# Kernel tuning notes

Hardware: AMD Instinct MI355X
Metric: run time of the kernel (lower is better)

Reference implementation:

```python
import jax, jax.numpy as jnp
import numpy as np
from jax import lax

WINDOW = 9
LOSS_WEIGHT = 1.0
EPS = 1e-05
BALANCE = 0.2

_DN = ('NCHW', 'OIHW', 'NCHW')

def _local_sum(x, k=WINDOW):
    # Separable box-filter sum == conv2d with ones((1,1,k,k)), padding=k//2.
    pad = k // 2
    kh = jnp.ones((1, 1, k, 1), x.dtype)
    kw = jnp.ones((1, 1, 1, k), x.dtype)
    y = lax.conv_general_dilated(x, kh, (1, 1), [(pad, pad), (0, 0)], dimension_numbers=_DN)
    return lax.conv_general_dilated(y, kw, (1, 1), [(0, 0), (pad, pad)], dimension_numbers=_DN)

def _lncc_loss(pred, target, k=WINDOW, eps=EPS):
    n = k * k
    pred_mean = _local_sum(pred, k) / n
    target_mean = _local_sum(target, k) / n
    # NOTE: faithful to source: variance uses raw local sum of squares minus mean^2
    pred_var = jnp.clip(_local_sum(pred * pred, k) - pred_mean * pred_mean, 0.0, None)
    target_var = jnp.clip(_local_sum(target * target, k) - target_mean * target_mean, 0.0, None)
    cov = _local_sum(pred * target, k) - pred_mean * target_mean
    lncc = cov / (jnp.sqrt(pred_var + eps) * jnp.sqrt(target_var + eps))
    return 1.0 - jnp.mean(lncc)

def setup_inputs() -> dict:
    key = jax.random.key(0)
    k1, k2, k3 = jax.random.split(key, 3)
    B, H, W = 16, 512, 512
    pred = jax.random.normal(k1, (B, 1, H, W), dtype=jnp.float32)
    target = jax.random.normal(k2, (B, 1, H, W), dtype=jnp.float32)
    mask = jax.random.normal(k3, (B, 2, H, W), dtype=jnp.float32)
    return {"pred": pred, "target": target, "mask": mask}

def reference(pred, target, mask):
    m = jnp.argmax(mask, axis=1)[:, None].astype(pred.dtype)  # [B,1,H,W]
    p_pred1 = (1.0 - m) * pred
    p_pred2 = (1.0 - m) * target
    n_pred1 = m * pred
    n_pred2 = m * target
    return LOSS_WEIGHT * (BALANCE * _lncc_loss(p_pred1, p_pred2)
                          - (1.0 - BALANCE) * _lncc_loss(n_pred1, n_pred2))
```

## Files before the change

### kernel.cpp

```cpp
#include <hip/hip_runtime.h>

#define NB   16
#define NH   512
#define NW   512
#define RAD  4
#define BH   4
#define NBANDS (NH / BH)
#define NBLOCKS (NB * NBANDS)
#define EPSF 1e-5f
#define SBYTES_PER_IMG (NH * NW / 8)
#define SBYTES_TOTAL   (NB * SBYTES_PER_IMG)

__device__ __forceinline__ float lncc_val(float Sa, float Sb, float Saa, float Sbb, float Sab) {
    const float inv_n = 1.0f / 81.0f;
    float ma  = Sa * inv_n;
    float mb  = Sb * inv_n;
    float va  = fmaxf(Saa - ma * ma, 0.0f);
    float vb  = fmaxf(Sbb - mb * mb, 0.0f);
    float cov = Sab - ma * mb;
    return cov * rsqrtf((va + EPSF) * (vb + EPSF));
}

__global__ __launch_bounds__(256)
void mask_pre(const float* __restrict__ mask, unsigned* __restrict__ sbits) {
    int tid = blockIdx.x * blockDim.x + threadIdx.x;
    const size_t hw = (size_t)NH * NW;
    size_t g0 = (size_t)tid * 32;
    int b = (int)(g0 / hw);
    size_t off = g0 - (size_t)b * hw;
    const float* c0 = mask + (size_t)b * 2 * hw + off;
    const float* c1 = c0 + hw;
    unsigned bits = 0;
    #pragma unroll
    for (int j = 0; j < 8; ++j) {
        float4 a  = *reinterpret_cast<const float4*>(c0 + j * 4);
        float4 bb = *reinterpret_cast<const float4*>(c1 + j * 4);
        bits |= (bb.x > a.x ? 1u : 0u) << (j * 4 + 0);
        bits |= (bb.y > a.y ? 1u : 0u) << (j * 4 + 1);
        bits |= (bb.z > a.z ? 1u : 0u) << (j * 4 + 2);
        bits |= (bb.w > a.w ? 1u : 0u) << (j * 4 + 3);
    }
    sbits[tid] = bits;
}

template<int SGN>
__device__ __forceinline__ void accum_row(const float* __restrict__ prow,
                                          const float* __restrict__ trow,
                                          const unsigned char* __restrict__ srow,
                                          int y, int lane,
                                          float (&V)[10][8])
{
    size_t off = (size_t)y * NW + lane * 8;
    float4 p0 = *reinterpret_cast<const float4*>(prow + off);
    float4 p1 = *reinterpret_cast<const float4*>(prow + off + 4);
    float4 t0 = *reinterpret_cast<const float4*>(trow + off);
    float4 t1 = *reinterpret_cast<const float4*>(trow + off + 4);
    unsigned bits = srow[y * (NW / 8) + lane];

    float p[8] = {p0.x,p0.y,p0.z,p0.w, p1.x,p1.y,p1.z,p1.w};
    float t[8] = {t0.x,t0.y,t0.z,t0.w, t1.x,t1.y,t1.z,t1.w};

    #pragma unroll
    for (int c = 0; c < 8; ++c) {
        float pv = p[c], tv = t[c];
        float s  = (float)((bits >> c) & 1u);
        if (SGN < 0) s = -s;
        float pp = pv * pv, tt = tv * tv, pt = pv * tv;
        if (SGN > 0) {
            V[0][c] += pv; V[1][c] += tv; V[2][c] += pp; V[3][c] += tt; V[4][c] += pt;
        } else {
            V[0][c] -= pv; V[1][c] -= tv; V[2][c] -= pp; V[3][c] -= tt; V[4][c] -= pt;
        }
        V[5][c] = fmaf(s, pv, V[5][c]); V[6][c] = fmaf(s, tv, V[6][c]);
        V[7][c] = fmaf(s, pp, V[7][c]); V[8][c] = fmaf(s, tt, V[8][c]);
        V[9][c] = fmaf(s, pt, V[9][c]);
    }
}

__global__ __launch_bounds__(64)
void lncc_main(const float* __restrict__ pred,
               const float* __restrict__ targ,
               const unsigned char* __restrict__ sbits,
               float* __restrict__ part)
{
    const int lane = threadIdx.x;
    const int b    = blockIdx.x / NBANDS;
    const int y0   = (blockIdx.x % NBANDS) * BH;

    const size_t hw   = (size_t)NH * NW;
    const float* prow = pred + (size_t)b * hw;
    const float* trow = targ + (size_t)b * hw;
    const unsigned char* srow = sbits + (size_t)b * SBYTES_PER_IMG;

    float V[10][8];
    #pragma unroll
    for (int q = 0; q < 10; ++q)
        #pragma unroll
        for (int c = 0; c < 8; ++c) V[q][c] = 0.0f;

    #pragma unroll
    for (int j = -RAD; j < RAD; ++j) {
        int y = y0 + j;
        if (y >= 0) accum_row<1>(prow, trow, srow, y, lane, V);
    }

    float sum_p = 0.0f, sum_n = 0.0f;

    #pragma clang loop unroll(disable)
    for (int r = 0; r < BH; ++r) {
        int y  = y0 + r;
        int ye = y + RAD;
        if (ye < NH) accum_row<1>(prow, trow, srow, ye, lane, V);

        {
            float Hh[10][4];
            #pragma unroll
            for (int q = 0; q < 10; ++q) {
                float hp0 = __shfl_up(V[q][4], 1);
                float hp1 = __shfl_up(V[q][5], 1);
                float hp2 = __shfl_up(V[q][6], 1);
                float hp3 = __shfl_up(V[q][7], 1);
                hp0 = (lane > 0) ? hp0 : 0.0f;
                hp1 = (lane > 0) ? hp1 : 0.0f;
                hp2 = (lane > 0) ? hp2 : 0.0f;
                hp3 = (lane > 0) ? hp3 : 0.0f;
                float h = ((hp0 + hp1) + (hp2 + hp3))
                        + ((V[q][0] + V[q][1]) + (V[q][2] + V[q][3])) + V[q][4];
                Hh[q][0] = h;
                h += V[q][5] - hp0; Hh[q][1] = h;
                h += V[q][6] - hp1; Hh[q][2] = h;
                h += V[q][7] - hp2; Hh[q][3] = h;
            }
            #pragma unroll
            for (int c = 0; c < 4; ++c) {
                float Sa=Hh[0][c], Sb=Hh[1][c], Saa=Hh[2][c], Sbb=Hh[3][c], Sab=Hh[4][c];
                float Ma=Hh[5][c], Mb=Hh[6][c], Maa=Hh[7][c], Mbb=Hh[8][c], Mab=Hh[9][c];
                sum_n += lncc_val(Ma, Mb, Maa, Mbb, Mab);
                sum_p += lncc_val(Sa-Ma, Sb-Mb, Saa-Maa, Sbb-Mbb, Sab-Mab);
            }
        }

        {
            float Hh[10][4];
            #pragma unroll
            for (int q = 0; q < 10; ++q) {
                float hn0 = __shfl_down(V[q][0], 1);
                float hn1 = __shfl_down(V[q][1], 1);
                float hn2 = __shfl_down(V[q][2], 1);
                float hn3 = __shfl_down(V[q][3], 1);
                hn0 = (lane < 63) ? hn0 : 0.0f;
                hn1 = (lane < 63) ? hn1 : 0.0f;
                hn2 = (lane < 63) ? hn2 : 0.0f;
                hn3 = (lane < 63) ? hn3 : 0.0f;
                float h = ((V[q][0] + V[q][1]) + (V[q][2] + V[q][3]))
                        + ((V[q][4] + V[q][5]) + (V[q][6] + V[q][7])) + hn0;
                Hh[q][0] = h;
                h += hn1 - V[q][0]; Hh[q][1] = h;
                h += hn2 - V[q][1]; Hh[q][2] = h;
                h += hn3 - V[q][2]; Hh[q][3] = h;
            }
            #pragma unroll
            for (int c = 0; c < 4; ++c) {
                float Sa=Hh[0][c], Sb=Hh[1][c], Saa=Hh[2][c], Sbb=Hh[3][c], Sab=Hh[4][c];
                float Ma=Hh[5][c], Mb=Hh[6][c], Maa=Hh[7][c], Mbb=Hh[8][c], Mab=Hh[9][c];
                sum_n += lncc_val(Ma, Mb, Maa, Mbb, Mab);
                sum_p += lncc_val(Sa-Ma, Sb-Mb, Saa-Maa, Sbb-Mbb, Sab-Mab);
            }
        }

        if (r < BH - 1) {
            int yl = y - RAD;
            if (yl >= 0) accum_row<-1>(prow, trow, srow, yl, lane, V);
        }
    }

    #pragma unroll
    for (int off = 32; off > 0; off >>= 1) {
        sum_p += __shfl_down(sum_p, off, 64);
        sum_n += __shfl_down(sum_n, off, 64);
    }
    if (lane == 0) {
        part[blockIdx.x]           = sum_p;
        part[NBLOCKS + blockIdx.x] = sum_n;
    }
}

__global__ void lncc_finalize(const float* __restrict__ part, float* __restrict__ out) {
    __shared__ float w[8];
    int tid = threadIdx.x;
    float sp = 0.0f, sn = 0.0f;
    for (int i = tid; i < NBLOCKS; i += 256) {
        sp += part[i];
        sn += part[NBLOCKS + i];
    }
    #pragma unroll
    for (int off = 32; off > 0; off >>= 1) {
        sp += __shfl_down(sp, off, 64);
        sn += __shfl_down(sn, off, 64);
    }
    int wave = tid >> 6, lane = tid & 63;
    if (lane == 0) { w[wave] = sp; w[4 + wave] = sn; }
    __syncthreads();
    if (tid == 0) {
        double SP = (double)w[0] + (double)w[1] + (double)w[2] + (double)w[3];
        double SN = (double)w[4] + (double)w[5] + (double)w[6] + (double)w[7];
        const double npix = (double)NB * (double)NH * (double)NW;
        double mp = SP / npix;
        double mn = SN / npix;
        out[0] = (float)(0.2 * (1.0 - mp) - 0.8 * (1.0 - mn));
    }
}

extern "C" void kernel_launch(void* const* d_in, const int* in_sizes, int n_in,
                              void* d_out, int out_size, void* d_ws, size_t ws_size,
                              hipStream_t stream) {
    const float* pred = (const float*)d_in[0];
    const float* targ = (const float*)d_in[1];
    const float* mask = (const float*)d_in[2];
    unsigned* sbits = (unsigned*)d_ws;
    float* part = (float*)((char*)d_ws + SBYTES_TOTAL);

    mask_pre<<<dim3(512), dim3(256), 0, stream>>>(mask, sbits);
    lncc_main<<<dim3(NBLOCKS), dim3(64), 0, stream>>>(pred, targ,
                                                      (const unsigned char*)sbits, part);
    lncc_finalize<<<dim3(1), dim3(256), 0, stream>>>(part, (float*)d_out);
}
```

Before: 129.3 us.

## Split each row across two waves with four columns per thread and LDS halo exchange

Measured after the change: 143.3 us. 10.8% more time.

```diff
diff --git a/kernel.cpp b/kernel.cpp
--- a/kernel.cpp
+++ b/kernel.cpp
@@ -7,6 +7,7 @@
 #define BH   4
 #define NBANDS (NH / BH)
 #define NBLOCKS (NB * NBANDS)
+#define NPART (NBLOCKS * 2)
 #define EPSF 1e-5f
 #define SBYTES_PER_IMG (NH * NW / 8)
 #define SBYTES_TOTAL   (NB * SBYTES_PER_IMG)
@@ -47,23 +48,22 @@
 __device__ __forceinline__ void accum_row(const float* __restrict__ prow,
                                           const float* __restrict__ trow,
                                           const unsigned char* __restrict__ srow,
-                                          int y, int lane,
-                                          float (&V)[10][8])
+                                          int y, int col0,
+                                          float (&V)[10][4])
 {
-    size_t off = (size_t)y * NW + lane * 8;
-    float4 p0 = *reinterpret_cast<const float4*>(prow + off);
-    float4 p1 = *reinterpret_cast<const float4*>(prow + off + 4);
-    float4 t0 = *reinterpret_cast<const float4*>(trow + off);
-    float4 t1 = *reinterpret_cast<const float4*>(trow + off + 4);
-    unsigned bits = srow[y * (NW / 8) + lane];
-
-    float p[8] = {p0.x,p0.y,p0.z,p0.w, p1.x,p1.y,p1.z,p1.w};
-    float t[8] = {t0.x,t0.y,t0.z,t0.w, t1.x,t1.y,t1.z,t1.w};
-
-    #pragma unroll
-    for (int c = 0; c < 8; ++c) {
+    size_t off = (size_t)y * NW + col0;
+    float4 pv4 = *reinterpret_cast<const float4*>(prow + off);
+    float4 tv4 = *reinterpret_cast<const float4*>(trow + off);
+    unsigned byte = srow[y * (NW / 8) + (col0 >> 3)];
+    unsigned nib  = (byte >> (col0 & 4)) & 0xFu;
+
+    float p[4] = {pv4.x, pv4.y, pv4.z, pv4.w};
+    float t[4] = {tv4.x, tv4.y, tv4.z, tv4.w};
+
+    #pragma unroll
+    for (int c = 0; c < 4; ++c) {
         float pv = p[c], tv = t[c];
-        float s  = (float)((bits >> c) & 1u);
+        float s  = (float)((nib >> c) & 1u);
         if (SGN < 0) s = -s;
         float pp = pv * pv, tt = tv * tv, pt = pv * tv;
         if (SGN > 0) {
@@ -77,13 +77,47 @@
     }
 }
 
-__global__ __launch_bounds__(64)
+__device__ __forceinline__ void horiz5(const float (&V)[10][4], int qbase,
+                                       int lane, int wv,
+                                       const float (*xl)[4], const float (*xr)[4],
+                                       float (&Hh)[5][4])
+{
+    #pragma unroll
+    for (int qi = 0; qi < 5; ++qi) {
+        const int q = qbase + qi;
+        float L0 = __shfl_up(V[q][0], 1), L1 = __shfl_up(V[q][1], 1);
+        float L2 = __shfl_up(V[q][2], 1), L3 = __shfl_up(V[q][3], 1);
+        if (lane == 0) {
+            if (wv == 1) { L0 = xl[q][0]; L1 = xl[q][1]; L2 = xl[q][2]; L3 = xl[q][3]; }
+            else         { L0 = L1 = L2 = L3 = 0.0f; }
+        }
+        float R0 = __shfl_down(V[q][0], 1), R1 = __shfl_down(V[q][1], 1);
+        float R2 = __shfl_down(V[q][2], 1), R3 = __shfl_down(V[q][3], 1);
+        if (lane == 63) {
+            if (wv == 0) { R0 = xr[q][0]; R1 = xr[q][1]; R2 = xr[q][2]; R3 = xr[q][3]; }
+            else         { R0 = R1 = R2 = R3 = 0.0f; }
+        }
+        float h = ((L0 + L1) + (L2 + L3))
+                + ((V[q][0] + V[q][1]) + (V[q][2] + V[q][3])) + R0;
+        Hh[qi][0] = h;
+        h += R1 - L0; Hh[qi][1] = h;
+        h += R2 - L1; Hh[qi][2] = h;
+        h += R3 - L2; Hh[qi][3] = h;
+    }
+}
+
+__global__ __launch_bounds__(128)
 void lncc_main(const float* __restrict__ pred,
                const float* __restrict__ targ,
                const unsigned char* __restrict__ sbits,
                float* __restrict__ part)
 {
-    const int lane = threadIdx.x;
+    __shared__ float xchg[2][2][10][4];
+
+    const int tid  = threadIdx.x;
+    const int lane = tid & 63;
+    const int wv   = tid >> 6;
+    const int col0 = tid * 4;
     const int b    = blockIdx.x / NBANDS;
     const int y0   = (blockIdx.x % NBANDS) * BH;
 
@@ -92,16 +126,16 @@
     const float* trow = targ + (size_t)b * hw;
     const unsigned char* srow = sbits + (size_t)b * SBYTES_PER_IMG;
 
-    float V[10][8];
+    float V[10][4];
     #pragma unroll
     for (int q = 0; q < 10; ++q)
         #pragma unroll
-        for (int c = 0; c < 8; ++c) V[q][c] = 0.0f;
+        for (int c = 0; c < 4; ++c) V[q][c] = 0.0f;
 
     #pragma unroll
     for (int j = -RAD; j < RAD; ++j) {
         int y = y0 + j;
-        if (y >= 0) accum_row<1>(prow, trow, srow, y, lane, V);
+        if (y >= 0) accum_row<1>(prow, trow, srow, y, col0, V);
     }
 
     float sum_p = 0.0f, sum_n = 0.0f;
@@ -110,67 +144,39 @@
     for (int r = 0; r < BH; ++r) {
         int y  = y0 + r;
         int ye = y + RAD;
-        if (ye < NH) accum_row<1>(prow, trow, srow, ye, lane, V);
-
-        {
-            float Hh[10][4];
+        if (ye < NH) accum_row<1>(prow, trow, srow, ye, col0, V);
+
+        float (*slot)[10][4] = xchg[r & 1];
+        if (tid == 63) {
             #pragma unroll
-            for (int q = 0; q < 10; ++q) {
-                float hp0 = __shfl_up(V[q][4], 1);
-                float hp1 = __shfl_up(V[q][5], 1);
-                float hp2 = __shfl_up(V[q][6], 1);
-                float hp3 = __shfl_up(V[q][7], 1);
-                hp0 = (lane > 0) ? hp0 : 0.0f;
-                hp1 = (lane > 0) ? hp1 : 0.0f;
-                hp2 = (lane > 0) ? hp2 : 0.0f;
-                hp3 = (lane > 0) ? hp3 : 0.0f;
-                float h = ((hp0 + hp1) + (hp2 + hp3))
-                        + ((V[q][0] + V[q][1]) + (V[q][2] + V[q][3])) + V[q][4];
-                Hh[q][0] = h;
-                h += V[q][5] - hp0; Hh[q][1] = h;
-                h += V[q][6] - hp1; Hh[q][2] = h;
-                h += V[q][7] - hp2; Hh[q][3] = h;
-            }
+            for (int q = 0; q < 10; ++q)
+                #pragma unroll
+                for (int c = 0; c < 4; ++c) slot[0][q][c] = V[q][c];
+        } else if (tid == 64) {
             #pragma unroll
-            for (int c = 0; c < 4; ++c) {
-                float Sa=Hh[0][c], Sb=Hh[1][c], Saa=Hh[2][c], Sbb=Hh[3][c], Sab=Hh[4][c];
-                float Ma=Hh[5][c], Mb=Hh[6][c], Maa=Hh[7][c], Mbb=Hh[8][c], Mab=Hh[9][c];
-                sum_n += lncc_val(Ma, Mb, Maa, Mbb, Mab);
-                sum_p += lncc_val(Sa-Ma, Sb-Mb, Saa-Maa, Sbb-Mbb, Sab-Mab);
-            }
-        }
-
-        {
-            float Hh[10][4];
-            #pragma unroll
-            for (int q = 0; q < 10; ++q) {
-                float hn0 = __shfl_down(V[q][0], 1);
-                float hn1 = __shfl_down(V[q][1], 1);
-                float hn2 = __shfl_down(V[q][2], 1);
-                float hn3 = __shfl_down(V[q][3], 1);
-                hn0 = (lane < 63) ? hn0 : 0.0f;
-                hn1 = (lane < 63) ? hn1 : 0.0f;
-                hn2 = (lane < 63) ? hn2 : 0.0f;
-                hn3 = (lane < 63) ? hn3 : 0.0f;
-                float h = ((V[q][0] + V[q][1]) + (V[q][2] + V[q][3]))
-                        + ((V[q][4] + V[q][5]) + (V[q][6] + V[q][7])) + hn0;
-                Hh[q][0] = h;
-                h += hn1 - V[q][0]; Hh[q][1] = h;
-                h += hn2 - V[q][1]; Hh[q][2] = h;
-                h += hn3 - V[q][2]; Hh[q][3] = h;
-            }
-            #pragma unroll
-            for (int c = 0; c < 4; ++c) {
-                float Sa=Hh[0][c], Sb=Hh[1][c], Saa=Hh[2][c], Sbb=Hh[3][c], Sab=Hh[4][c];
-                float Ma=Hh[5][c], Mb=Hh[6][c], Maa=Hh[7][c], Mbb=Hh[8][c], Mab=Hh[9][c];
-                sum_n += lncc_val(Ma, Mb, Maa, Mbb, Mab);
-                sum_p += lncc_val(Sa-Ma, Sb-Mb, Saa-Maa, Sbb-Mbb, Sab-Mab);
-            }
-        }
+            for (int q = 0; q < 10; ++q)
+                #pragma unroll
+                for (int c = 0; c < 4; ++c) slot[1][q][c] = V[q][c];
+        }
+        __syncthreads();
+
+        float Mh[5][4];
+        horiz5(V, 5, lane, wv, slot[0], slot[1], Mh);
+        #pragma unroll
+        for (int c = 0; c < 4; ++c)
+            sum_n += lncc_val(Mh[0][c], Mh[1][c], Mh[2][c], Mh[3][c], Mh[4][c]);
+
+        float Sh[5][4];
+        horiz5(V, 0, lane, wv, slot[0], slot[1], Sh);
+        #pragma unroll
+        for (int c = 0; c < 4; ++c)
+            sum_p += lncc_val(Sh[0][c] - Mh[0][c], Sh[1][c] - Mh[1][c],
+                              Sh[2][c] - Mh[2][c], Sh[3][c] - Mh[3][c],
+                              Sh[4][c] - Mh[4][c]);
 
         if (r < BH - 1) {
             int yl = y - RAD;
-            if (yl >= 0) accum_row<-1>(prow, trow, srow, yl, lane, V);
+            if (yl >= 0) accum_row<-1>(prow, trow, srow, yl, col0, V);
         }
     }
 
@@ -180,8 +186,9 @@
         sum_n += __shfl_down(sum_n, off, 64);
     }
     if (lane == 0) {
-        part[blockIdx.x]           = sum_p;
-        part[NBLOCKS + blockIdx.x] = sum_n;
+        int idx = blockIdx.x * 2 + wv;
+        part[idx]         = sum_p;
+        part[NPART + idx] = sum_n;
     }
 }
 
@@ -189,9 +196,9 @@
     __shared__ float w[8];
     int tid = threadIdx.x;
     float sp = 0.0f, sn = 0.0f;
-    for (int i = tid; i < NBLOCKS; i += 256) {
+    for (int i = tid; i < NPART; i += 256) {
         sp += part[i];
-        sn += part[NBLOCKS + i];
+        sn += part[NPART + i];
     }
     #pragma unroll
     for (int off = 32; off > 0; off >>= 1) {
@@ -221,7 +228,7 @@
     float* part = (float*)((char*)d_ws + SBYTES_TOTAL);
 
     mask_pre<<<dim3(512), dim3(256), 0, stream>>>(mask, sbits);
-    lncc_main<<<dim3(NBLOCKS), dim3(64), 0, stream>>>(pred, targ,
-                                                      (const unsigned char*)sbits, part);
+    lncc_main<<<dim3(NBLOCKS), dim3(128), 0, stream>>>(pred, targ,
+                                                       (const unsigned char*)sbits, part);
     lncc_finalize<<<dim3(1), dim3(256), 0, stream>>>(part, (float*)d_out);
 }
```
